# Optimization experiments

Hardware: AMD Instinct MI355X
Metric: run time of the kernel (lower is better)

The kernel has to match this reference:

```python
import jax, jax.numpy as jnp
import numpy as np

N = 200000   # num nodes
E = 600000   # num edges (avg fan-in 3)
D = 128      # dim_hidden
DX = 3       # dim_node_feature
DM = 256     # dim_mlp
DP = 1       # dim_pred
NUM_LEVELS = 16
NUM_ROUNDS = 1


def setup_inputs() -> dict:
    key = jax.random.key(0)
    k = jax.random.split(key, 12)
    s = lambda fan: 1.0 / np.sqrt(fan).astype(np.float32)
    return {
        "x": jax.random.normal(k[0], (N, DX), jnp.float32),
        "edge_index": jax.random.randint(k[1], (2, E), 0, N, dtype=jnp.int32),
        "forward_level": jax.random.randint(k[2], (N,), 0, NUM_LEVELS, dtype=jnp.int32),
        # emd_int: Linear(1, D) applied to the constant 1.0
        "W_emd": jax.random.normal(k[3], (D, 1), jnp.float32),
        "b_emd": jax.random.normal(k[4], (D,), jnp.float32) * 0.1,
        # conv_sum aggregation pre-mlp: Linear(D, D)
        "W_aggr": jax.random.normal(k[5], (D, D), jnp.float32) * s(D),
        "b_aggr": jnp.zeros((D,), jnp.float32),
        # GRU(D+DX, D) weights, torch layout (gates r,z,n stacked)
        "w_ih": jax.random.normal(k[6], (3 * D, D + DX), jnp.float32) * s(D + DX),
        "w_hh": jax.random.normal(k[7], (3 * D, D), jnp.float32) * s(D),
        "b_ih": jnp.zeros((3 * D,), jnp.float32),
        "b_hh": jnp.zeros((3 * D,), jnp.float32),
        # predictor MLP: D -> DM -> DM -> DP with ReLU
        "W1": jax.random.normal(k[8], (DM, D), jnp.float32) * s(D),
        "b1": jnp.zeros((DM,), jnp.float32),
        "W2": jax.random.normal(k[9], (DM, DM), jnp.float32) * s(DM),
        "b2": jnp.zeros((DM,), jnp.float32),
        "W3": jax.random.normal(k[10], (DP, DM), jnp.float32) * s(DM),
        "b3": jnp.zeros((DP,), jnp.float32),
    }


def reference(x, edge_index, forward_level, W_emd, b_emd, W_aggr, b_aggr,
              w_ih, w_hh, b_ih, b_hh, W1, b1, W2, b2, W3, b3):
    src, dst = edge_index[0], edge_index[1]
    dst_level = forward_level[dst]  # [E]

    # h_init = emd_int(1.0), broadcast to every node
    h = jnp.broadcast_to(W_emd[:, 0] + b_emd, (N, D))

    def level_step(h, l):
        # conv_sum aggregation: mlp on source states, sum-scatter to dst,
        # restricted to the level-l subgraph (edges whose dst is at level l).
        t = h @ W_aggr.T + b_aggr                          # [N, D]
        emask = (dst_level == l).astype(h.dtype)           # [E]
        msg = jax.ops.segment_sum(t[src] * emask[:, None], dst, num_segments=N)
        # GRU cell update (torch gate order r, z, n); wx_update -> input [msg, x]
        inp = jnp.concatenate([msg, x], axis=1)            # [N, D+DX]
        gi = inp @ w_ih.T + b_ih
        gh = h @ w_hh.T + b_hh
        r = jax.nn.sigmoid(gi[:, :D] + gh[:, :D])
        z = jax.nn.sigmoid(gi[:, D:2 * D] + gh[:, D:2 * D])
        n = jnp.tanh(gi[:, 2 * D:] + r * gh[:, 2 * D:])
        h_new = (1.0 - z) * n + z * h
        # only nodes at level l get the new state
        nmask = (forward_level == l)[:, None]
        return jnp.where(nmask, h_new, h), None

    for _ in range(NUM_ROUNDS):
        h, _ = jax.lax.scan(level_step, h, jnp.arange(1, NUM_LEVELS))

    # predictor MLP (num_fc=3, ReLU, no norm)
    h1 = jax.nn.relu(h @ W1.T + b1)
    h2 = jax.nn.relu(h1 @ W2.T + b2)
    return h2 @ W3.T + b3
```

## Files before the change

kernel.cpp:

```cpp
#include <hip/hip_runtime.h>

#define NN 200000
#define NE 600000
#define DD 128
#define DXX 3
#define DMM 256
#define NLVL 16

#define OFF_H      0LL
#define OFF_CSO    102400000LL
#define OFF_DEG    103200016LL
#define OFF_CUR    104000016LL
#define OFF_CSRC   104800016LL
#define OFF_BSUM   107200016LL
#define OFF_NLIST  107201040LL
#define OFF_WCH    108001040LL
#define OFF_GHC    108099344LL
#define OFF_MB     108100880LL
#define OFF_W1H    108102416LL
#define OFF_W2H    108167952LL
#define OFF_CNT    108299024LL
#define WS_NEEDED  108299536LL


typedef float    f32x4 __attribute__((ext_vector_type(4)));
typedef _Float16 f16x8 __attribute__((ext_vector_type(8)));

__device__ __forceinline__ float sigm(float x){
  x = fminf(fmaxf(x, -30.f), 30.f);
  return 1.f/(1.f + __expf(-x));
}
__device__ __forceinline__ float tanh_(float x){
  x = fminf(fmaxf(x, -15.f), 15.f);
  float e = __expf(2.f*x);
  return (e - 1.f)/(e + 1.f);
}

__global__ void k_init_h(_Float16* h16, const int* fl,
                         const float* W_emd, const float* b_emd){
  __shared__ _Float16 h0f[DD];
  if (threadIdx.x < DD) h0f[threadIdx.x] = (_Float16)(W_emd[threadIdx.x] + b_emd[threadIdx.x]);
  __syncthreads();
  const int tot = NN*16;
  for (int i = blockIdx.x*blockDim.x + threadIdx.x; i < tot; i += gridDim.x*blockDim.x){
    int row = i >> 4, ch = i & 15;
    if (fl[row] == 0)
      *(f16x8*)(h16 + (size_t)row*DD + ch*8) = *(const f16x8*)&h0f[ch*8];
  }
}

__global__ void k_count(const int* fl, int* cnt){
  __shared__ int hn[NLVL];
  if (threadIdx.x < NLVL) hn[threadIdx.x] = 0;
  __syncthreads();
  for (int i = blockIdx.x*blockDim.x + threadIdx.x; i < NN; i += gridDim.x*blockDim.x)
    atomicAdd(&hn[fl[i]], 1);
  __syncthreads();
  if (threadIdx.x < NLVL && hn[threadIdx.x])
    atomicAdd(&cnt[threadIdx.x], hn[threadIdx.x]);
}

__global__ void k_scan(int* cnt){
  if (threadIdx.x == 0){
    int s = 0;
    for (int l=0;l<NLVL;l++){ cnt[32+l] = s; s += cnt[l]; }
    cnt[48] = s;
    for (int l=0;l<NLVL;l++) cnt[66+l] = 0;
  }
}

#define FB 1024
__global__ __launch_bounds__(256) void k_fill_n(const int* fl, int* cnt, int* node_list){
  __shared__ int hist[NLVL], base[NLVL];
  const int nt = (NN + FB - 1)/FB;
  for (int tile = blockIdx.x; tile < nt; tile += gridDim.x){
    const int i0 = tile*FB;
    if (threadIdx.x < NLVL) hist[threadIdx.x] = 0;
    __syncthreads();
    int lv[4], rk[4];
    #pragma unroll
    for (int j=0;j<4;j++){
      int i = i0 + threadIdx.x + j*256;
      if (i < NN){
        int l = fl[i];
        lv[j] = l;
        rk[j] = atomicAdd(&hist[l], 1);
      } else lv[j] = -1;
    }
    __syncthreads();
    if (threadIdx.x < NLVL)
      base[threadIdx.x] = atomicAdd(&cnt[66+threadIdx.x], hist[threadIdx.x]);
    __syncthreads();
    #pragma unroll
    for (int j=0;j<4;j++){
      if (lv[j] >= 0){
        int i = i0 + threadIdx.x + j*256;
        node_list[cnt[32+lv[j]] + base[lv[j]] + rk[j]] = i;
      }
    }
    __syncthreads();
  }
}

__global__ void k_deg(const int* dst, int* deg){
  for (int e = blockIdx.x*blockDim.x + threadIdx.x; e < NE; e += gridDim.x*blockDim.x)
    atomicAdd(&deg[dst[e]], 1);
}

#define SCB 1024
__global__ __launch_bounds__(1024) void k_cscan1(const int* deg, int* cso, int* bsum){
  __shared__ int sh[SCB];
  const int b = blockIdx.x, t = threadIdx.x;
  const int i = b*SCB + t;
  int v = (i < NN) ? deg[i] : 0;
  sh[t] = v;
  __syncthreads();
  for (int ofs=1; ofs<SCB; ofs<<=1){
    int add = (t >= ofs) ? sh[t-ofs] : 0;
    __syncthreads();
    sh[t] += add;
    __syncthreads();
  }
  if (i < NN) cso[i] = sh[t] - v;
  if (t == SCB-1) bsum[b] = sh[t];
}
__global__ void k_cscan2(int* bsum, int* cso, int nb){
  if (threadIdx.x == 0){
    int run = 0;
    for (int b=0;b<nb;b++){ int tmp = bsum[b]; bsum[b] = run; run += tmp; }
    cso[NN] = run;
  }
}
__global__ __launch_bounds__(1024) void k_cscan3(int* cso, const int* bsum){
  const int i = blockIdx.x*SCB + threadIdx.x;
  if (i < NN) cso[i] += bsum[blockIdx.x];
}

__global__ void k_csr_fill(const int* srcp, const int* dstp, const int* fl,
                           const int* cso, int* cur, int* csr_pack){
  for (int e = blockIdx.x*blockDim.x + threadIdx.x; e < NE; e += gridDim.x*blockDim.x){
    int d = dstp[e];
    int s = srcp[e];
    int p = atomicAdd(&cur[d], 1);
    csr_pack[cso[d] + p] = s | (fl[s] << 24);
  }
}

__global__ void k_prep(const float* w_ih, const float* W_aggr, const float* b_aggr,
                       const float* w_hh, const float* W_emd, const float* b_emd,
                       const float* b_hh, const float* W1, const float* W2,
                       _Float16* Wch, float* ghc, float* mb,
                       _Float16* W1h, _Float16* W2h){
  const int tid = blockIdx.x*blockDim.x + threadIdx.x;
  const int stride = gridDim.x*blockDim.x;
  for (int i = tid; i < 384*DD; i += stride){
    int r = i >> 7, k = i & (DD-1);
    float s = 0.f;
    for (int j=0;j<DD;j++) s += w_ih[r*(DD+DXX)+j]*W_aggr[j*DD+k];
    Wch[i] = (_Float16)s;
  }
  for (int i = tid; i < 384; i += stride){
    float s = 0.f, gg = 0.f;
    for (int j=0;j<DD;j++){
      s  += w_ih[i*(DD+DXX)+j]*b_aggr[j];
      gg += w_hh[i*DD+j]*(W_emd[j] + b_emd[j]);
    }
    mb[i]  = s;
    ghc[i] = gg + b_hh[i];
  }
  for (int i = tid; i < DMM*DD;  i += stride) W1h[i] = (_Float16)W1[i];
  for (int i = tid; i < DMM*DMM; i += stride) W2h[i] = (_Float16)W2[i];
}

#define GT 32
__global__ __launch_bounds__(512, 4) void k_level_one(const int* cnt, const int l,
    const int* node_list, const int* cso, const int* csr_pack,
    const float* x, const _Float16* Wch, const float* ghc, const float* mb,
    const float* w_ih, const float* b_ih, const float* W_emd, const float* b_emd,
    _Float16* h16){
  const int n0 = cnt[32+l];
  const int na = cnt[32+l+1] - n0;
  const int tb = blockIdx.x * GT;
  if (tb >= na) return;

  __shared__ float s_l[GT][DD+4];
  __shared__ float x_l[GT][4];
  __shared__ float deg_l[GT];
  __shared__ int   vidx[GT], eoff[GT], ecnt[GT];
  __shared__ float h0s[DD];
  const int t    = threadIdx.x;
  const int w    = t >> 6;
  const int lane = t & 63;
  const int c0   = lane & 15;
  const int g    = lane >> 4;
  const int jo   = w*16 + c0;

  if (t < DD) h0s[t] = W_emd[t] + b_emd[t];
  if (t < GT){
    int row = tb + t;
    int v = (row < na) ? node_list[n0 + row] : -1;
    vidx[t] = v;
    int e0 = 0, e1 = 0;
    if (v >= 0){ e0 = cso[v]; e1 = cso[v+1]; }
    eoff[t] = e0; ecnt[t] = e1 - e0;
    deg_l[t] = (float)(e1 - e0);
    for (int kx=0; kx<DXX; kx++) x_l[t][kx] = (v >= 0) ? x[v*DXX + kx] : 0.f;
  }

  f16x8 wcf[3][4];
  #pragma unroll
  for (int gate = 0; gate < 3; gate++){
    const _Float16* wp = Wch + (size_t)(gate*128 + jo)*DD + 8*g;
    #pragma unroll
    for (int ks = 0; ks < 4; ks++) wcf[gate][ks] = *(const f16x8*)(wp + ks*32);
  }
  float biv[3], mbv[3], ghcv[3], wxv[3][3];
  #pragma unroll
  for (int gate = 0; gate < 3; gate++){
    biv[gate]  = b_ih[gate*128 + jo];
    mbv[gate]  = mb[gate*128 + jo];
    ghcv[gate] = ghc[gate*128 + jo];
    #pragma unroll
    for (int kx = 0; kx < 3; kx++)
      wxv[gate][kx] = w_ih[(size_t)(gate*128 + jo)*(DD+DXX) + DD + kx];
  }
  const float h0v = W_emd[jo] + b_emd[jo];
  __syncthreads();

  {
    const int j = t >> 4, sub = t & 15;
    const int v = vidx[j];
    float acc[8] = {0,0,0,0,0,0,0,0};
    int nh0 = 0;
    if (v >= 0){
      const int e0 = eoff[j], n = ecnt[j];
      int i = 0;
      for (; i + 1 < n; i += 2){
        int pk0 = csr_pack[e0+i], pk1 = csr_pack[e0+i+1];
        int f0 = pk0 >> 24, f1 = pk1 >> 24;
        bool d0 = (f0 != 0) & (f0 < l);
        bool d1 = (f1 != 0) & (f1 < l);
        f16x8 v0, v1;
        if (d0) v0 = *(const f16x8*)(h16 + (size_t)(pk0 & 0xFFFFFF)*DD + sub*8); else nh0++;
        if (d1) v1 = *(const f16x8*)(h16 + (size_t)(pk1 & 0xFFFFFF)*DD + sub*8); else nh0++;
        if (d0){
          #pragma unroll
          for (int q=0;q<8;q++) acc[q] += (float)v0[q];
        }
        if (d1){
          #pragma unroll
          for (int q=0;q<8;q++) acc[q] += (float)v1[q];
        }
      }
      if (i < n){
        int pk = csr_pack[e0+i];
        int fv = pk >> 24;
        if (fv && fv < l){
          f16x8 vv = *(const f16x8*)(h16 + (size_t)(pk & 0xFFFFFF)*DD + sub*8);
          #pragma unroll
          for (int q=0;q<8;q++) acc[q] += (float)vv[q];
        } else nh0++;
      }
      if (nh0){
        float nh = (float)nh0;
        #pragma unroll
        for (int q=0;q<8;q++) acc[q] += nh*h0s[sub*8+q];
      }
    }
    *(float4*)&s_l[j][sub*8]     = make_float4(acc[0],acc[1],acc[2],acc[3]);
    *(float4*)&s_l[j][sub*8 + 4] = make_float4(acc[4],acc[5],acc[6],acc[7]);
  }
  __syncthreads();

  #pragma unroll
  for (int m = 0; m < 2; m++){
    const int a_row = m*16 + c0;
    f16x8 as[4];
    #pragma unroll
    for (int ks = 0; ks < 4; ks++){
      const float* sp = &s_l[a_row][ks*32 + 8*g];
      f16x8 av;
      #pragma unroll
      for (int i2 = 0; i2 < 8; i2++) av[i2] = (_Float16)sp[i2];
      as[ks] = av;
    }
    f32x4 gi[3];
    #pragma unroll
    for (int gate = 0; gate < 3; gate++) gi[gate] = (f32x4){0.f,0.f,0.f,0.f};
    #pragma unroll
    for (int gate = 0; gate < 3; gate++)
      #pragma unroll
      for (int ks = 0; ks < 4; ks++)
        gi[gate] = __builtin_amdgcn_mfma_f32_16x16x32_f16(as[ks], wcf[gate][ks], gi[gate], 0, 0, 0);
    #pragma unroll
    for (int r = 0; r < 4; r++){
      const int node = m*16 + 4*g + r;
      const int v = vidx[node];
      if (v < 0) continue;
      const float dg = deg_l[node];
      float xr = 0.f, xz = 0.f, xn = 0.f;
      #pragma unroll
      for (int kx = 0; kx < 3; kx++){
        float xv = x_l[node][kx];
        xr = fmaf(wxv[0][kx], xv, xr);
        xz = fmaf(wxv[1][kx], xv, xz);
        xn = fmaf(wxv[2][kx], xv, xn);
      }
      float grv = gi[0][r] + biv[0] + dg*mbv[0] + xr + ghcv[0];
      float gzv = gi[1][r] + biv[1] + dg*mbv[1] + xz + ghcv[1];
      float rr = sigm(grv);
      float zz = sigm(gzv);
      float gnv = gi[2][r] + biv[2] + dg*mbv[2] + xn + rr*ghcv[2];
      float nv = tanh_(gnv);
      h16[(size_t)v*DD + jo] = (_Float16)((1.f - zz)*nv + zz*h0v);
    }
  }
}

__global__ __launch_bounds__(1024, 1) void k_mlp_pw(const _Float16* __restrict__ h16,
    const _Float16* __restrict__ W1h, const float* __restrict__ b1,
    const _Float16* __restrict__ W2h, const float* __restrict__ b2,
    const float* __restrict__ W3, const float* __restrict__ b3,
    float* __restrict__ out){
  __shared__ _Float16 hA[64*128];
  __shared__ _Float16 h1s[64*256];
  __shared__ float red[16][64];
  const int t    = threadIdx.x;
  const int w    = t >> 6;
  const int lane = t & 63;
  const int c    = lane & 15;
  const int g    = lane >> 4;
  const int col  = w*16 + c;

  f16x8 w1f[4], w2f[8];
  #pragma unroll
  for (int s = 0; s < 4; s++) w1f[s] = *(const f16x8*)(W1h + (size_t)col*DD  + s*32 + 8*g);
  #pragma unroll
  for (int s = 0; s < 8; s++) w2f[s] = *(const f16x8*)(W2h + (size_t)col*DMM + s*32 + 8*g);
  const float bb1 = b1[col], bb2 = b2[col], w3v = W3[col], b3s = b3[0];

  for (int tile = blockIdx.x; tile < NN/64; tile += gridDim.x){
    const int base = tile*64;
    {
      int byte = t*16;
      int row  = byte >> 8;
      int swz  = byte ^ ((row & 7) << 4);
      *(f16x8*)((char*)hA + swz) = ((const f16x8*)(h16 + (size_t)base*DD))[t];
    }
    __syncthreads();

    f32x4 acc[4];
    #pragma unroll
    for (int m = 0; m < 4; m++){
      acc[m] = (f32x4){0.f,0.f,0.f,0.f};
      int row = m*16 + c;
      #pragma unroll
      for (int s = 0; s < 4; s++){
        int byte = row*256 + ((g*16 + s*64) ^ ((row & 7) << 4));
        f16x8 a1 = *(const f16x8*)((const char*)hA + byte);
        acc[m] = __builtin_amdgcn_mfma_f32_16x16x32_f16(a1, w1f[s], acc[m], 0, 0, 0);
      }
    }
    #pragma unroll
    for (int m = 0; m < 4; m++)
      #pragma unroll
      for (int r = 0; r < 4; r++){
        int row = m*16 + 4*g + r;
        int off = (row*512 + col*2) ^ ((row & 7) << 4);
        *(_Float16*)((char*)h1s + off) = (_Float16)fmaxf(acc[m][r] + bb1, 0.f);
      }
    __syncthreads();

    float p[4][4];
    #pragma unroll
    for (int m = 0; m < 4; m++){
      int row = m*16 + c;
      f16x8 a2[8];
      #pragma unroll
      for (int s = 0; s < 8; s++){
        int off = (row*512 + s*64 + g*16) ^ ((row & 7) << 4);
        a2[s] = *(const f16x8*)((const char*)h1s + off);
      }
      f32x4 acc2 = (f32x4){0.f,0.f,0.f,0.f};
      #pragma unroll
      for (int s = 0; s < 8; s++)
        acc2 = __builtin_amdgcn_mfma_f32_16x16x32_f16(a2[s], w2f[s], acc2, 0, 0, 0);
      #pragma unroll
      for (int r = 0; r < 4; r++)
        p[m][r] = fmaxf(acc2[r] + bb2, 0.f) * w3v;
    }
    #pragma unroll
    for (int msk = 1; msk < 16; msk <<= 1)
      #pragma unroll
      for (int m = 0; m < 4; m++)
        #pragma unroll
        for (int r = 0; r < 4; r++)
          p[m][r] += __shfl_xor(p[m][r], msk);
    if (c == 0){
      #pragma unroll
      for (int m = 0; m < 4; m++)
        #pragma unroll
        for (int r = 0; r < 4; r++)
          red[w][m*16 + 4*g + r] = p[m][r];
    }
    __syncthreads();
    if (t < 64){
      float s = b3s;
      #pragma unroll
      for (int j = 0; j < 16; j++) s += red[j][t];
      out[base + t] = s;
    }
    __syncthreads();
  }
}

extern "C" void kernel_launch(void* const* d_in, const int* in_sizes, int n_in,
                              void* d_out, int out_size, void* d_ws, size_t ws_size,
                              hipStream_t stream){
  if (ws_size < (size_t)WS_NEEDED) return;
  const float* x      = (const float*)d_in[0];
  const int*   ei     = (const int*)  d_in[1];
  const int*   srcp   = ei;
  const int*   dstp   = ei + NE;
  const int*   fl     = (const int*)  d_in[2];
  const float* W_emd  = (const float*)d_in[3];
  const float* b_emd  = (const float*)d_in[4];
  const float* W_aggr = (const float*)d_in[5];
  const float* b_aggr = (const float*)d_in[6];
  const float* w_ih   = (const float*)d_in[7];
  const float* w_hh   = (const float*)d_in[8];
  const float* b_ih   = (const float*)d_in[9];
  const float* b_hh   = (const float*)d_in[10];
  const float* W1     = (const float*)d_in[11];
  const float* b1     = (const float*)d_in[12];
  const float* W2     = (const float*)d_in[13];
  const float* b2     = (const float*)d_in[14];
  const float* W3     = (const float*)d_in[15];
  const float* b3     = (const float*)d_in[16];

  char* ws = (char*)d_ws;
  _Float16* h16   = (_Float16*)(ws + OFF_H);
  int*   cso      = (int*)  (ws + OFF_CSO);
  int*   deg      = (int*)  (ws + OFF_DEG);
  int*   cur      = (int*)  (ws + OFF_CUR);
  int*   csr_pack = (int*)  (ws + OFF_CSRC);
  int*   bsum     = (int*)  (ws + OFF_BSUM);
  int*   node_list= (int*)  (ws + OFF_NLIST);
  _Float16* Wch   = (_Float16*)(ws + OFF_WCH);
  float* ghc      = (float*)(ws + OFF_GHC);
  float* mb       = (float*)(ws + OFF_MB);
  _Float16* W1h   = (_Float16*)(ws + OFF_W1H);
  _Float16* W2h   = (_Float16*)(ws + OFF_W2H);
  int*   cnt      = (int*)  (ws + OFF_CNT);
  float* outp     = (float*)d_out;

  const int nsb = (NN + SCB - 1)/SCB;

  hipMemsetAsync(ws + OFF_CNT, 0, 512, stream);
  hipMemsetAsync(ws + OFF_DEG, 0, 1600000, stream);
  k_init_h<<<2048, 256, 0, stream>>>(h16, fl, W_emd, b_emd);
  k_count<<<1024, 256, 0, stream>>>(fl, cnt);
  k_scan<<<1, 64, 0, stream>>>(cnt);
  k_fill_n<<<196, 256, 0, stream>>>(fl, cnt, node_list);
  k_deg<<<1024, 256, 0, stream>>>(dstp, deg);
  k_cscan1<<<nsb, SCB, 0, stream>>>(deg, cso, bsum);
  k_cscan2<<<1, 64, 0, stream>>>(bsum, cso, nsb);
  k_cscan3<<<nsb, SCB, 0, stream>>>(cso, bsum);
  k_csr_fill<<<1024, 256, 0, stream>>>(srcp, dstp, fl, cso, cur, csr_pack);
  k_prep<<<256, 256, 0, stream>>>(w_ih, W_aggr, b_aggr, w_hh, W_emd, b_emd, b_hh,
                                  W1, W2, Wch, ghc, mb, W1h, W2h);
  for (int l = 1; l < NLVL; l++)
    k_level_one<<<512, 512, 0, stream>>>(cnt, l, node_list, cso, csr_pack, x,
                                         Wch, ghc, mb, w_ih, b_ih, W_emd, b_emd, h16);
  k_mlp_pw<<<256, 1024, 0, stream>>>(h16, W1h, b1, W2h, b2, W3, b3, outp);
}
```

Measured before the change: 509.0 us.

## Fuse setup kernels, unroll gather by four, double MLP occupancy and grid

```diff
diff --git a/kernel.cpp b/kernel.cpp
--- a/kernel.cpp
+++ b/kernel.cpp
@@ -35,26 +35,26 @@
   float e = __expf(2.f*x);
   return (e - 1.f)/(e + 1.f);
 }
-
-__global__ void k_init_h(_Float16* h16, const int* fl,
-                         const float* W_emd, const float* b_emd){
+__device__ __forceinline__ void acc8(float* acc, f16x8 v){
+  for (int q = 0; q < 8; q++) acc[q] += (float)v[q];
+}
+
+__global__ void k_pre(_Float16* h16, const int* fl, const int* dst,
+                      const float* W_emd, const float* b_emd, int* cnt, int* deg){
+  __shared__ int hn[NLVL];
   __shared__ _Float16 h0f[DD];
+  if (threadIdx.x < NLVL) hn[threadIdx.x] = 0;
   if (threadIdx.x < DD) h0f[threadIdx.x] = (_Float16)(W_emd[threadIdx.x] + b_emd[threadIdx.x]);
   __syncthreads();
-  const int tot = NN*16;
-  for (int i = blockIdx.x*blockDim.x + threadIdx.x; i < tot; i += gridDim.x*blockDim.x){
+  const int tid = blockIdx.x*blockDim.x + threadIdx.x;
+  const int stride = gridDim.x*blockDim.x;
+  for (int i = tid; i < NN*16; i += stride){
     int row = i >> 4, ch = i & 15;
     if (fl[row] == 0)
       *(f16x8*)(h16 + (size_t)row*DD + ch*8) = *(const f16x8*)&h0f[ch*8];
   }
-}
-
-__global__ void k_count(const int* fl, int* cnt){
-  __shared__ int hn[NLVL];
-  if (threadIdx.x < NLVL) hn[threadIdx.x] = 0;
-  __syncthreads();
-  for (int i = blockIdx.x*blockDim.x + threadIdx.x; i < NN; i += gridDim.x*blockDim.x)
-    atomicAdd(&hn[fl[i]], 1);
+  for (int i = tid; i < NN; i += stride) atomicAdd(&hn[fl[i]], 1);
+  for (int e = tid; e < NE; e += stride) atomicAdd(&deg[dst[e]], 1);
   __syncthreads();
   if (threadIdx.x < NLVL && hn[threadIdx.x])
     atomicAdd(&cnt[threadIdx.x], hn[threadIdx.x]);
@@ -100,11 +100,6 @@
     }
     __syncthreads();
   }
-}
-
-__global__ void k_deg(const int* dst, int* deg){
-  for (int e = blockIdx.x*blockDim.x + threadIdx.x; e < NE; e += gridDim.x*blockDim.x)
-    atomicAdd(&deg[dst[e]], 1);
 }
 
 #define SCB 1024
@@ -124,13 +119,39 @@
   if (i < NN) cso[i] = sh[t] - v;
   if (t == SCB-1) bsum[b] = sh[t];
 }
-__global__ void k_cscan2(int* bsum, int* cso, int nb){
-  if (threadIdx.x == 0){
+
+__global__ void k_cscan2_prep(int* bsum, int* cso, int nb,
+                       const float* w_ih, const float* W_aggr, const float* b_aggr,
+                       const float* w_hh, const float* W_emd, const float* b_emd,
+                       const float* b_hh, const float* W1, const float* W2,
+                       _Float16* Wch, float* ghc, float* mb,
+                       _Float16* W1h, _Float16* W2h){
+  if (blockIdx.x == 0 && threadIdx.x == 0){
     int run = 0;
     for (int b=0;b<nb;b++){ int tmp = bsum[b]; bsum[b] = run; run += tmp; }
     cso[NN] = run;
   }
-}
+  const int tid = blockIdx.x*blockDim.x + threadIdx.x;
+  const int stride = gridDim.x*blockDim.x;
+  for (int i = tid; i < 384*DD; i += stride){
+    int r = i >> 7, k = i & (DD-1);
+    float s = 0.f;
+    for (int j=0;j<DD;j++) s += w_ih[r*(DD+DXX)+j]*W_aggr[j*DD+k];
+    Wch[i] = (_Float16)s;
+  }
+  for (int i = tid; i < 384; i += stride){
+    float s = 0.f, gg = 0.f;
+    for (int j=0;j<DD;j++){
+      s  += w_ih[i*(DD+DXX)+j]*b_aggr[j];
+      gg += w_hh[i*DD+j]*(W_emd[j] + b_emd[j]);
+    }
+    mb[i]  = s;
+    ghc[i] = gg + b_hh[i];
+  }
+  for (int i = tid; i < DMM*DD;  i += stride) W1h[i] = (_Float16)W1[i];
+  for (int i = tid; i < DMM*DMM; i += stride) W2h[i] = (_Float16)W2[i];
+}
+
 __global__ __launch_bounds__(1024) void k_cscan3(int* cso, const int* bsum){
   const int i = blockIdx.x*SCB + threadIdx.x;
   if (i < NN) cso[i] += bsum[blockIdx.x];
@@ -144,32 +165,6 @@
     int p = atomicAdd(&cur[d], 1);
     csr_pack[cso[d] + p] = s | (fl[s] << 24);
   }
-}
-
-__global__ void k_prep(const float* w_ih, const float* W_aggr, const float* b_aggr,
-                       const float* w_hh, const float* W_emd, const float* b_emd,
-                       const float* b_hh, const float* W1, const float* W2,
-                       _Float16* Wch, float* ghc, float* mb,
-                       _Float16* W1h, _Float16* W2h){
-  const int tid = blockIdx.x*blockDim.x + threadIdx.x;
-  const int stride = gridDim.x*blockDim.x;
-  for (int i = tid; i < 384*DD; i += stride){
-    int r = i >> 7, k = i & (DD-1);
-    float s = 0.f;
-    for (int j=0;j<DD;j++) s += w_ih[r*(DD+DXX)+j]*W_aggr[j*DD+k];
-    Wch[i] = (_Float16)s;
-  }
-  for (int i = tid; i < 384; i += stride){
-    float s = 0.f, gg = 0.f;
-    for (int j=0;j<DD;j++){
-      s  += w_ih[i*(DD+DXX)+j]*b_aggr[j];
-      gg += w_hh[i*DD+j]*(W_emd[j] + b_emd[j]);
-    }
-    mb[i]  = s;
-    ghc[i] = gg + b_hh[i];
-  }
-  for (int i = tid; i < DMM*DD;  i += stride) W1h[i] = (_Float16)W1[i];
-  for (int i = tid; i < DMM*DMM; i += stride) W2h[i] = (_Float16)W2[i];
 }
 
 #define GT 32
@@ -235,35 +230,43 @@
     if (v >= 0){
       const int e0 = eoff[j], n = ecnt[j];
       int i = 0;
-      for (; i + 1 < n; i += 2){
-        int pk0 = csr_pack[e0+i], pk1 = csr_pack[e0+i+1];
-        int f0 = pk0 >> 24, f1 = pk1 >> 24;
-        bool d0 = (f0 != 0) & (f0 < l);
-        bool d1 = (f1 != 0) & (f1 < l);
-        f16x8 v0, v1;
-        if (d0) v0 = *(const f16x8*)(h16 + (size_t)(pk0 & 0xFFFFFF)*DD + sub*8); else nh0++;
-        if (d1) v1 = *(const f16x8*)(h16 + (size_t)(pk1 & 0xFFFFFF)*DD + sub*8); else nh0++;
-        if (d0){
-          #pragma unroll
-          for (int q=0;q<8;q++) acc[q] += (float)v0[q];
-        }
-        if (d1){
-          #pragma unroll
-          for (int q=0;q<8;q++) acc[q] += (float)v1[q];
-        }
-      }
-      if (i < n){
-        int pk = csr_pack[e0+i];
-        int fv = pk >> 24;
-        if (fv && fv < l){
-          f16x8 vv = *(const f16x8*)(h16 + (size_t)(pk & 0xFFFFFF)*DD + sub*8);
-          #pragma unroll
-          for (int q=0;q<8;q++) acc[q] += (float)vv[q];
-        } else nh0++;
+      for (; i + 4 <= n; i += 4){
+        int p0 = csr_pack[e0+i+0];
+        int p1 = csr_pack[e0+i+1];
+        int p2 = csr_pack[e0+i+2];
+        int p3 = csr_pack[e0+i+3];
+        int f0=p0>>24, f1=p1>>24, f2=p2>>24, f3=p3>>24;
+        bool d0=(f0!=0)&(f0<l), d1=(f1!=0)&(f1<l), d2=(f2!=0)&(f2<l), d3=(f3!=0)&(f3<l);
+        f16x8 v0, v1, v2, v3;
+        if (d0) v0 = *(const f16x8*)(h16 + (size_t)(p0 & 0xFFFFFF)*DD + sub*8); else nh0++;
+        if (d1) v1 = *(const f16x8*)(h16 + (size_t)(p1 & 0xFFFFFF)*DD + sub*8); else nh0++;
+        if (d2) v2 = *(const f16x8*)(h16 + (size_t)(p2 & 0xFFFFFF)*DD + sub*8); else nh0++;
+        if (d3) v3 = *(const f16x8*)(h16 + (size_t)(p3 & 0xFFFFFF)*DD + sub*8); else nh0++;
+        if (d0) acc8(acc, v0);
+        if (d1) acc8(acc, v1);
+        if (d2) acc8(acc, v2);
+        if (d3) acc8(acc, v3);
+      }
+      const int r = n - i;
+      if (r > 0){
+        int p0 = csr_pack[e0+i];
+        int p1 = (r > 1) ? csr_pack[e0+i+1] : 0;
+        int p2 = (r > 2) ? csr_pack[e0+i+2] : 0;
+        int f0=p0>>24, f1=p1>>24, f2=p2>>24;
+        bool d0=(f0!=0)&(f0<l);
+        bool d1=(r>1)&(f1!=0)&(f1<l);
+        bool d2=(r>2)&(f2!=0)&(f2<l);
+        f16x8 v0, v1, v2;
+        if (d0) v0 = *(const f16x8*)(h16 + (size_t)(p0 & 0xFFFFFF)*DD + sub*8);
+        if (d1) v1 = *(const f16x8*)(h16 + (size_t)(p1 & 0xFFFFFF)*DD + sub*8);
+        if (d2) v2 = *(const f16x8*)(h16 + (size_t)(p2 & 0xFFFFFF)*DD + sub*8);
+        nh0 += (d0?0:1) + ((r>1)?(d1?0:1):0) + ((r>2)?(d2?0:1):0);
+        if (d0) acc8(acc, v0);
+        if (d1) acc8(acc, v1);
+        if (d2) acc8(acc, v2);
       }
       if (nh0){
         float nh = (float)nh0;
-        #pragma unroll
         for (int q=0;q<8;q++) acc[q] += nh*h0s[sub*8+q];
       }
     }
@@ -317,7 +320,7 @@
   }
 }
 
-__global__ __launch_bounds__(1024, 1) void k_mlp_pw(const _Float16* __restrict__ h16,
+__global__ __launch_bounds__(1024, 2) void k_mlp_pw(const _Float16* __restrict__ h16,
     const _Float16* __restrict__ W1h, const float* __restrict__ b1,
     const _Float16* __restrict__ W2h, const float* __restrict__ b2,
     const float* __restrict__ W3, const float* __restrict__ b3,
@@ -456,21 +459,19 @@
 
   const int nsb = (NN + SCB - 1)/SCB;
 
-  hipMemsetAsync(ws + OFF_CNT, 0, 512, stream);
-  hipMemsetAsync(ws + OFF_DEG, 0, 1600000, stream);
-  k_init_h<<<2048, 256, 0, stream>>>(h16, fl, W_emd, b_emd);
-  k_count<<<1024, 256, 0, stream>>>(fl, cnt);
+  (void)hipMemsetAsync(ws + OFF_CNT, 0, 512, stream);
+  (void)hipMemsetAsync(ws + OFF_DEG, 0, 1600000, stream);
+  k_pre<<<2048, 256, 0, stream>>>(h16, fl, dstp, W_emd, b_emd, cnt, deg);
   k_scan<<<1, 64, 0, stream>>>(cnt);
   k_fill_n<<<196, 256, 0, stream>>>(fl, cnt, node_list);
-  k_deg<<<1024, 256, 0, stream>>>(dstp, deg);
   k_cscan1<<<nsb, SCB, 0, stream>>>(deg, cso, bsum);
-  k_cscan2<<<1, 64, 0, stream>>>(bsum, cso, nsb);
+  k_cscan2_prep<<<256, 256, 0, stream>>>(bsum, cso, nsb,
+                                  w_ih, W_aggr, b_aggr, w_hh, W_emd, b_emd, b_hh,
+                                  W1, W2, Wch, ghc, mb, W1h, W2h);
   k_cscan3<<<nsb, SCB, 0, stream>>>(cso, bsum);
   k_csr_fill<<<1024, 256, 0, stream>>>(srcp, dstp, fl, cso, cur, csr_pack);
-  k_prep<<<256, 256, 0, stream>>>(w_ih, W_aggr, b_aggr, w_hh, W_emd, b_emd, b_hh,
-                                  W1, W2, Wch, ghc, mb, W1h, W2h);
   for (int l = 1; l < NLVL; l++)
     k_level_one<<<512, 512, 0, stream>>>(cnt, l, node_list, cso, csr_pack, x,
                                          Wch, ghc, mb, w_ih, b_ih, W_emd, b_emd, h16);
-  k_mlp_pw<<<256, 1024, 0, stream>>>(h16, W1h, b1, W2h, b2, W3, b3, outp);
-}
+  k_mlp_pw<<<512, 1024, 0, stream>>>(h16, W1h, b1, W2h, b2, W3, b3, outp);
+}
```

Measured after the change: 500.2 us. About the same (-1.7%).
